# Performance work log

Hardware: AMD Instinct MI355X
Metric: run time of the kernel (lower is better)

Reference implementation:

```python
import jax, jax.numpy as jnp
import numpy as np

EPS_NORM = 1e-12   # F.normalize eps
EPS_Q = 1e-5       # quant scale clamp

def simple_rmsnorm(x):
    # F.normalize(x, dim=-1) * sqrt(dim)  ==  x / sqrt(mean(x^2))
    d = x.shape[-1]
    n = jnp.maximum(jnp.linalg.norm(x, axis=-1, keepdims=True), EPS_NORM)
    return x / n * jnp.sqrt(jnp.asarray(d, x.dtype))

def activation_quant(x):
    # per-token 8-bit absmax quant
    scale = 127.0 / jnp.clip(jnp.max(jnp.abs(x), axis=-1, keepdims=True), EPS_Q, None)
    return jnp.clip(jnp.round(x * scale), -128.0, 127.0) / scale

def weight_quant(w):
    # per-tensor ternary quant: scale = 1 / mean|w|
    scale = 1.0 / jnp.clip(jnp.mean(jnp.abs(w)), EPS_Q, None)
    return jnp.clip(jnp.round(w * scale), -1.0, 1.0) / scale

def bitlinear158(x, w):
    xn = simple_rmsnorm(x)
    # straight-through estimators
    xq = xn + jax.lax.stop_gradient(activation_quant(xn) - xn)
    wq = w + jax.lax.stop_gradient(weight_quant(w) - w)
    # w is [out, in] like nn.Linear
    return jnp.einsum('bsd,od->bso', xq, wq)

def setup_inputs() -> dict:
    key = jax.random.key(0)
    k1, k2, k3 = jax.random.split(key, 3)
    dim, inner = 2048, 8192
    x = jax.random.normal(k1, (4, 2048, dim), dtype=jnp.float32)
    w1 = jax.random.normal(k2, (inner, dim), dtype=jnp.float32) * 0.02
    w2 = jax.random.normal(k3, (dim, inner), dtype=jnp.float32) * 0.02
    return {"x": x, "w1": w1, "w2": w2}

def reference(x, w1, w2):
    h = bitlinear158(x, w1)
    h = jax.nn.gelu(h, approximate=False)  # nn.GELU() default = exact erf
    return bitlinear158(h, w2)
```

## Files before the change

### kernel.cpp

```cpp
#include <hip/hip_runtime.h>
#include <hip/hip_bf16.h>
#include <hip/hip_fp16.h>

typedef __attribute__((ext_vector_type(4))) int i32x4;
typedef __attribute__((ext_vector_type(8))) unsigned short u16x8;
typedef __attribute__((ext_vector_type(8))) char c8;
typedef __attribute__((ext_vector_type(4))) char c4;
typedef unsigned int u32;
typedef unsigned short u16;

#define SCH0() __builtin_amdgcn_sched_barrier(0)

__device__ __forceinline__ void gload_lds16(const void* g, void* l) {
  __builtin_amdgcn_global_load_lds((const u32 __attribute__((address_space(1)))*)g,
                                   (u32 __attribute__((address_space(3)))*)l, 16, 0, 0);
}
__device__ __forceinline__ float h2f(u16 u) { return __half2float(__ushort_as_half(u)); }
__device__ __forceinline__ u16  f2h(float f){ return __half_as_ushort(__float2half_rn(f)); }

__global__ __launch_bounds__(256) void prep_kernel(const float* __restrict__ x,
    char* __restrict__ qx, float* __restrict__ invs,
    const float* __restrict__ w1, const float* __restrict__ w2,
    double* __restrict__ part) {
  const int tid = threadIdx.x;
  __shared__ double sd[256];
  __shared__ float sf[256];
  if (blockIdx.x < 8192) {
    const int D = 2048;
    int row = blockIdx.x;
    const float* xr = x + (size_t)row * D;
    float4 a = ((const float4*)xr)[tid * 2], b = ((const float4*)xr)[tid * 2 + 1];
    float v[8] = {a.x, a.y, a.z, a.w, b.x, b.y, b.z, b.w};
    double ss = 0; float mx = 0.0f;
#pragma unroll
    for (int i = 0; i < 8; i++) { ss += (double)v[i] * v[i]; mx = fmaxf(mx, fabsf(v[i])); }
    sd[tid] = ss; sf[tid] = mx; __syncthreads();
    for (int o = 128; o > 0; o >>= 1) {
      if (tid < o) { sd[tid] += sd[tid + o]; sf[tid] = fmaxf(sf[tid], sf[tid + o]); }
      __syncthreads();
    }
    __shared__ float bn, bs;
    if (tid == 0) {
      float n = fmaxf((float)sqrt(sd[0]), 1e-12f);
      float amax = sf[0] * (sqrtf((float)D) / n);
      float cl = fmaxf(amax, 1e-5f);
      bn = n; bs = 127.0f / cl;
      invs[row] = cl / 127.0f;
    }
    __syncthreads();
    float n = bn, s = bs, sq = sqrtf((float)D);
    c8 q;
#pragma unroll
    for (int i = 0; i < 8; i++) {
      float xn = (v[i] / n) * sq;
      float r = rintf(xn * s);
      r = fminf(fmaxf(r, -128.0f), 127.0f);
      q[i] = (char)(int)r;
    }
    *(c8*)&qx[(size_t)row * D + tid * 8] = q;
  } else {
    const int n4 = 4194304;
    const bool isw2 = blockIdx.x >= 8704;
    const float* w = isw2 ? w2 : w1;
    const int vb = blockIdx.x - (isw2 ? 8704 : 8192);
    double s = 0;
    for (int i = vb * 256 + tid; i < n4; i += 512 * 256) {
      float4 v = ((const float4*)w)[i];
      s += (double)fabsf(v.x) + (double)fabsf(v.y) + (double)fabsf(v.z) + (double)fabsf(v.w);
    }
    sd[tid] = s; __syncthreads();
    for (int o = 128; o > 0; o >>= 1) { if (tid < o) sd[tid] += sd[tid + o]; __syncthreads(); }
    if (tid == 0) part[(isw2 ? 512 : 0) + vb] = sd[0];
  }
}

__global__ __launch_bounds__(256) void wscale_final(const double* __restrict__ part,
    float* __restrict__ wsc) {
  int tid = threadIdx.x;
  __shared__ double sd[256];
  sd[tid] = part[tid] + part[tid + 256]; __syncthreads();
  for (int o = 128; o > 0; o >>= 1) { if (tid < o) sd[tid] += sd[tid + o]; __syncthreads(); }
  double s1 = sd[0]; __syncthreads();
  sd[tid] = part[512 + tid] + part[768 + tid]; __syncthreads();
  for (int o = 128; o > 0; o >>= 1) { if (tid < o) sd[tid] += sd[tid + o]; __syncthreads(); }
  if (tid == 0) {
    float m1 = (float)(s1 / 16777216.0);
    float m2 = (float)(sd[0] / 16777216.0);
    float d1 = fmaxf(m1, 1e-5f), d2 = fmaxf(m2, 1e-5f);
    wsc[0] = 1.0f / d1; wsc[1] = d1; wsc[2] = 1.0f / d2; wsc[3] = d2;
  }
}

__global__ __launch_bounds__(256) void quant_w_kernel(const float* __restrict__ w1,
    char* __restrict__ q1, const float* __restrict__ w2, char* __restrict__ q2,
    const float* __restrict__ wsc) {
  const int n4 = 4194304;
  const bool isw2 = blockIdx.x >= 2048;
  const float* w = isw2 ? w2 : w1;
  char* q = isw2 ? q2 : q1;
  float s = isw2 ? wsc[2] : wsc[0];
  const int vb = blockIdx.x - (isw2 ? 2048 : 0);
  for (int i = vb * 256 + threadIdx.x; i < n4; i += 2048 * 256) {
    float4 v = ((const float4*)w)[i];
    c4 o;
    o[0] = (char)(int)(fminf(fmaxf(rintf(v.x * s), -1.0f), 1.0f));
    o[1] = (char)(int)(fminf(fmaxf(rintf(v.y * s), -1.0f), 1.0f));
    o[2] = (char)(int)(fminf(fmaxf(rintf(v.z * s), -1.0f), 1.0f));
    o[3] = (char)(int)(fminf(fmaxf(rintf(v.w * s), -1.0f), 1.0f));
    ((c4*)q)[i] = o;
  }
}

#define READ_A3(BUF, HALF, DST)                                            \
  { _Pragma("unroll") for (int f_ = 0; f_ < 4; f_++)                       \
      DST[f_] = *(const i32x4*)&sm[BUF][0][(wm * 128 + (HALF) * 64 + llo + f_ * 16) * 64 + koff]; }
#define READ_B3(BUF, HALF, DST)                                            \
  { _Pragma("unroll") for (int f_ = 0; f_ < 2; f_++)                       \
      DST[f_] = *(const i32x4*)&sm[BUF][1][(wn * 64 + (HALF) * 32 + llo + f_ * 16) * 64 + koff]; }
#define MMAQ(AV, BV, MH, NH)                                               \
  { __builtin_amdgcn_s_setprio(1);                                         \
    _Pragma("unroll") for (int m_ = 0; m_ < 4; m_++)                       \
      _Pragma("unroll") for (int n_ = 0; n_ < 2; n_++)                     \
        acc[(MH) * 4 + m_][(NH) * 2 + n_] =                                \
            __builtin_amdgcn_mfma_i32_16x16x64_i8(AV[m_], BV[n_],          \
                acc[(MH) * 4 + m_][(NH) * 2 + n_], 0, 0, 0);               \
    __builtin_amdgcn_s_setprio(0); }
#define STAGE3(BUF, KT)                                                    \
  { size_t ko_ = (size_t)(KT) * 64;                                        \
    gload_lds16(gA0 + ko_, &sm[BUF][0][tid * 16]);                         \
    gload_lds16(gB0 + ko_, &sm[BUF][1][tid * 16]);                         \
    gload_lds16(gA1 + ko_, &sm[BUF][0][8192 + tid * 16]);                  \
    gload_lds16(gB1 + ko_, &sm[BUF][1][8192 + tid * 16]); }
#define TILE_M(BR, BN, BS, KT)                                             \
  { STAGE3(BS, (KT) + 2);                                                  \
    SCH0();                                                                \
    READ_B3(BR, 1, bhi); SCH0();                                           \
    MMAQ(alo, blo, 0, 0); SCH0();                                          \
    READ_A3(BR, 1, ahi); SCH0();                                           \
    MMAQ(alo, bhi, 0, 1);                                                  \
    MMAQ(ahi, blo, 1, 0); SCH0();                                          \
    asm volatile("s_waitcnt vmcnt(4) lgkmcnt(0)\n\ts_barrier" ::: "memory"); \
    READ_A3(BN, 0, alo); READ_B3(BN, 0, blo); SCH0();                      \
    MMAQ(ahi, bhi, 1, 1); }

template <int EPI>
__global__ __launch_bounds__(512, 2) void gemm_i8(const char* __restrict__ A,
    const char* __restrict__ B, int N, int K, size_t ldA, size_t ldB, int gridN,
    const float* __restrict__ rowscale, const float* __restrict__ wsc,
    int widx, void* __restrict__ outp) {
  __shared__ __align__(16) char sm[3][2][16384];
  const int tid = threadIdx.x;
  const int lane = tid & 63, w = tid >> 6;
  const int wm = w >> 2, wn = w & 3;
  const int llo = lane & 15, lhi = lane >> 4;
  const int koff = ((lhi ^ ((llo >> 1) & 3)) << 4);

  const int nwg = gridDim.x, cpx = nwg >> 3;
  const int swz = (blockIdx.x & 7) * cpx + (blockIdx.x >> 3);
  const int band = gridN << 2;
  const int g = swz / band, idx = swz % band;
  const int bm = (g << 2) + (idx & 3), bn = idx >> 2;

  const int NT = K >> 6;
  const int NITER = (NT - 2) / 3;

  const int rs = tid >> 2;
  const int kbs = (((tid & 3) ^ ((tid >> 3) & 3)) << 4);
  const char* gA0 = A + (size_t)(bm * 256 + rs) * ldA + kbs;
  const char* gA1 = gA0 + (size_t)128 * ldA;
  const char* gB0 = B + (size_t)(bn * 256 + rs) * ldB + kbs;
  const char* gB1 = gB0 + (size_t)128 * ldB;

  i32x4 alo[4], ahi[4], blo[2], bhi[2];
  i32x4 acc[8][4];
#pragma unroll
  for (int m = 0; m < 8; m++)
#pragma unroll
    for (int n = 0; n < 4; n++) acc[m][n] = (i32x4){0, 0, 0, 0};

  STAGE3(0, 0);
  asm volatile("s_nop 0" ::: "memory");
  STAGE3(1, 1);
  asm volatile("s_waitcnt vmcnt(4)\n\ts_barrier" ::: "memory");
  READ_A3(0, 0, alo); READ_B3(0, 0, blo);

  for (int it = 0, t = 0; it < NITER; ++it, t += 3) {
    TILE_M(0, 1, 2, t);
    TILE_M(1, 2, 0, t + 1);
    TILE_M(2, 0, 1, t + 2);
  }
  {
    SCH0();
    READ_B3(0, 1, bhi); SCH0();
    MMAQ(alo, blo, 0, 0); SCH0();
    READ_A3(0, 1, ahi); SCH0();
    MMAQ(alo, bhi, 0, 1);
    MMAQ(ahi, blo, 1, 0); SCH0();
    asm volatile("s_waitcnt vmcnt(0) lgkmcnt(0)\n\ts_barrier" ::: "memory");
    READ_A3(1, 0, alo); READ_B3(1, 0, blo); SCH0();
    MMAQ(ahi, bhi, 1, 1);
  }
  {
    READ_B3(1, 1, bhi);
    MMAQ(alo, blo, 0, 0);
    READ_A3(1, 1, ahi);
    MMAQ(alo, bhi, 0, 1);
    MMAQ(ahi, blo, 1, 0);
    MMAQ(ahi, bhi, 1, 1);
  }

  float wdeq = wsc[widx];
#pragma unroll
  for (int mf = 0; mf < 8; mf++) {
#pragma unroll
    for (int reg = 0; reg < 4; reg++) {
      int r = bm * 256 + wm * 128 + mf * 16 + lhi * 4 + reg;
      float deq = rowscale[r] * wdeq;
#pragma unroll
      for (int nf = 0; nf < 4; nf++) {
        int c = bn * 256 + wn * 64 + nf * 16 + llo;
        float val = (float)acc[mf][nf][reg] * deq;
        if (EPI == 0) {
          float gg = 0.5f * val * (1.0f + erff(val * 0.70710678118654752440f));
          ((u16*)outp)[(size_t)r * N + c] = f2h(gg);
        } else {
          ((float*)outp)[(size_t)r * N + c] = val;
        }
      }
    }
  }
}

__global__ __launch_bounds__(256) void quant_h_kernel(u16* __restrict__ h, float* __restrict__ invs) {
  const int D = 8192;
  int row = blockIdx.x, tid = threadIdx.x;
  u16* hr = h + (size_t)row * D;
  float v[32];
#pragma unroll
  for (int j = 0; j < 4; j++) {
    u16x8 u = *(const u16x8*)&hr[j * 2048 + tid * 8];
#pragma unroll
    for (int e = 0; e < 8; e++) v[j * 8 + e] = h2f(u[e]);
  }
  double ss = 0; float mx = 0.0f;
#pragma unroll
  for (int i = 0; i < 32; i++) { ss += (double)v[i] * v[i]; mx = fmaxf(mx, fabsf(v[i])); }
  __shared__ double sd[256]; __shared__ float sf[256];
  sd[tid] = ss; sf[tid] = mx; __syncthreads();
  for (int o = 128; o > 0; o >>= 1) {
    if (tid < o) { sd[tid] += sd[tid + o]; sf[tid] = fmaxf(sf[tid], sf[tid + o]); }
    __syncthreads();
  }
  __shared__ float bn, bs;
  if (tid == 0) {
    float n = fmaxf((float)sqrt(sd[0]), 1e-12f);
    float amax = sf[0] * (sqrtf((float)D) / n);
    float cl = fmaxf(amax, 1e-5f);
    bn = n; bs = 127.0f / cl;
    invs[row] = cl / 127.0f;
  }
  __syncthreads();
  float n = bn, s = bs, sq = sqrtf((float)D);
  char* hq = (char*)hr;
#pragma unroll
  for (int j = 0; j < 4; j++) {
    c8 q;
#pragma unroll
    for (int e = 0; e < 8; e++) {
      float xn = (v[j * 8 + e] / n) * sq;
      float r = rintf(xn * s);
      r = fminf(fmaxf(r, -128.0f), 127.0f);
      q[e] = (char)(int)r;
    }
    *(c8*)&hq[j * 2048 + tid * 8] = q;
  }
}

extern "C" void kernel_launch(void* const* d_in, const int* in_sizes, int n_in,
                              void* d_out, int out_size, void* d_ws, size_t ws_size,
                              hipStream_t stream) {
  const float* x  = (const float*)d_in[0];
  const float* w1 = (const float*)d_in[1];
  const float* w2 = (const float*)d_in[2];

  char* ws = (char*)d_ws;
  char*   qx     = (char*)(ws + 0);
  char*   w1q    = (char*)(ws + 16777216);
  char*   w2q    = (char*)(ws + 33554432);
  u16*    h      = (u16*)(ws + 50331648);
  float*  invs_x = (float*)(ws + 184549376);
  float*  invs_h = (float*)(ws + 184582144);
  double* part   = (double*)(ws + 184614912);
  float*  wsc    = (float*)(ws + 184623104);

  prep_kernel<<<9216, 256, 0, stream>>>(x, qx, invs_x, w1, w2, part);
  wscale_final<<<1, 256, 0, stream>>>(part, wsc);
  quant_w_kernel<<<4096, 256, 0, stream>>>(w1, w1q, w2, w2q, wsc);
  gemm_i8<0><<<1024, 512, 0, stream>>>(qx, w1q, 8192, 2048, 2048, 2048, 32,
                                       invs_x, wsc, 1, (void*)h);
  quant_h_kernel<<<8192, 256, 0, stream>>>(h, invs_h);
  gemm_i8<1><<<256, 512, 0, stream>>>((const char*)h, w2q, 2048, 8192, 16384, 8192, 8,
                                      invs_h, wsc, 3, d_out);
}
```

Measured before the change: 421.7 us.

## Switch int8 GEMM to double-buffered 128-wide K tiles with 8-way swizzle

The int8 GEMM main loop moves from a triple-buffered 64-byte K step (prefetching two tiles ahead) to a double-buffered 128-byte K step that prefetches one tile ahead. The LDS swizzle widens from 4 to 8 16-byte chunks per row. The aim is to halve the number of barriers and loop iterations and to issue larger global-to-LDS copies. In exchange, each barrier waits on vmcnt(0), so the copy of the next tile has less time to overlap with compute, and LDS use grows from 96 KB to 128 KB per block.

Result: slower. 452.3 us (+7.3%).

```diff
diff --git a/kernel.cpp b/kernel.cpp
--- a/kernel.cpp
+++ b/kernel.cpp
@@ -111,36 +111,49 @@
   }
 }
 
-#define READ_A3(BUF, HALF, DST)                                            \
-  { _Pragma("unroll") for (int f_ = 0; f_ < 4; f_++)                       \
-      DST[f_] = *(const i32x4*)&sm[BUF][0][(wm * 128 + (HALF) * 64 + llo + f_ * 16) * 64 + koff]; }
-#define READ_B3(BUF, HALF, DST)                                            \
-  { _Pragma("unroll") for (int f_ = 0; f_ < 2; f_++)                       \
-      DST[f_] = *(const i32x4*)&sm[BUF][1][(wn * 64 + (HALF) * 32 + llo + f_ * 16) * 64 + koff]; }
-#define MMAQ(AV, BV, MH, NH)                                               \
-  { __builtin_amdgcn_s_setprio(1);                                         \
-    _Pragma("unroll") for (int m_ = 0; m_ < 4; m_++)                       \
-      _Pragma("unroll") for (int n_ = 0; n_ < 2; n_++)                     \
-        acc[(MH) * 4 + m_][(NH) * 2 + n_] =                                \
-            __builtin_amdgcn_mfma_i32_16x16x64_i8(AV[m_], BV[n_],          \
-                acc[(MH) * 4 + m_][(NH) * 2 + n_], 0, 0, 0);               \
+#define RD_A128(BUF, H, S, DST)                                             \
+  { _Pragma("unroll") for (int f_ = 0; f_ < 4; f_++)                        \
+      DST[f_] = *(const i32x4*)&sm[BUF][0][(wm * 128 + (H) * 64 + llo + f_ * 16) * 128 \
+                                           + (((((S) << 2) + lhi) ^ sw) << 4)]; }
+#define RD_B128(BUF, H, S, DST)                                             \
+  { _Pragma("unroll") for (int f_ = 0; f_ < 2; f_++)                        \
+      DST[f_] = *(const i32x4*)&sm[BUF][1][(wn * 64 + (H) * 32 + llo + f_ * 16) * 128 \
+                                           + (((((S) << 2) + lhi) ^ sw) << 4)]; }
+#define MMAQ(AV, BV, MH, NH)                                                \
+  { __builtin_amdgcn_s_setprio(1);                                          \
+    _Pragma("unroll") for (int m_ = 0; m_ < 4; m_++)                        \
+      _Pragma("unroll") for (int n_ = 0; n_ < 2; n_++)                      \
+        acc[(MH) * 4 + m_][(NH) * 2 + n_] =                                 \
+            __builtin_amdgcn_mfma_i32_16x16x64_i8(AV[m_], BV[n_],           \
+                acc[(MH) * 4 + m_][(NH) * 2 + n_], 0, 0, 0);                \
     __builtin_amdgcn_s_setprio(0); }
-#define STAGE3(BUF, KT)                                                    \
-  { size_t ko_ = (size_t)(KT) * 64;                                        \
-    gload_lds16(gA0 + ko_, &sm[BUF][0][tid * 16]);                         \
-    gload_lds16(gB0 + ko_, &sm[BUF][1][tid * 16]);                         \
-    gload_lds16(gA1 + ko_, &sm[BUF][0][8192 + tid * 16]);                  \
-    gload_lds16(gB1 + ko_, &sm[BUF][1][8192 + tid * 16]); }
-#define TILE_M(BR, BN, BS, KT)                                             \
-  { STAGE3(BS, (KT) + 2);                                                  \
-    SCH0();                                                                \
-    READ_B3(BR, 1, bhi); SCH0();                                           \
-    MMAQ(alo, blo, 0, 0); SCH0();                                          \
-    READ_A3(BR, 1, ahi); SCH0();                                           \
-    MMAQ(alo, bhi, 0, 1);                                                  \
-    MMAQ(ahi, blo, 1, 0); SCH0();                                          \
-    asm volatile("s_waitcnt vmcnt(4) lgkmcnt(0)\n\ts_barrier" ::: "memory"); \
-    READ_A3(BN, 0, alo); READ_B3(BN, 0, blo); SCH0();                      \
+#define STAGE128(BUF, KT)                                                   \
+  { size_t ko_ = (size_t)(KT) * 128;                                        \
+    gload_lds16(gA0 + ko_, &sm[BUF][0][tid * 16]);                          \
+    gload_lds16(gA1 + ko_, &sm[BUF][0][tid * 16 + 8192]);                   \
+    gload_lds16(gA2 + ko_, &sm[BUF][0][tid * 16 + 16384]);                  \
+    gload_lds16(gA3 + ko_, &sm[BUF][0][tid * 16 + 24576]);                  \
+    gload_lds16(gB0 + ko_, &sm[BUF][1][tid * 16]);                          \
+    gload_lds16(gB1 + ko_, &sm[BUF][1][tid * 16 + 8192]);                   \
+    gload_lds16(gB2 + ko_, &sm[BUF][1][tid * 16 + 16384]);                  \
+    gload_lds16(gB3 + ko_, &sm[BUF][1][tid * 16 + 24576]); }
+#define TILE128(C, T)                                                       \
+  { asm volatile("s_waitcnt vmcnt(0) lgkmcnt(0)\n\ts_barrier" ::: "memory");\
+    if ((T) + 1 < NT) STAGE128(C ^ 1, (T) + 1);                             \
+    SCH0();                                                                 \
+    RD_A128(C, 0, 0, alo); RD_B128(C, 0, 0, blo);                           \
+    RD_B128(C, 1, 0, bhi); SCH0();                                          \
+    MMAQ(alo, blo, 0, 0); SCH0();                                           \
+    RD_A128(C, 1, 0, ahi); SCH0();                                          \
+    MMAQ(alo, bhi, 0, 1);                                                   \
+    MMAQ(ahi, blo, 1, 0); SCH0();                                           \
+    RD_A128(C, 0, 1, alo); RD_B128(C, 0, 1, blo); SCH0();                   \
+    MMAQ(ahi, bhi, 1, 1);                                                   \
+    RD_B128(C, 1, 1, bhi); SCH0();                                          \
+    MMAQ(alo, blo, 0, 0); SCH0();                                           \
+    RD_A128(C, 1, 1, ahi); SCH0();                                          \
+    MMAQ(alo, bhi, 0, 1);                                                   \
+    MMAQ(ahi, blo, 1, 0); SCH0();                                           \
     MMAQ(ahi, bhi, 1, 1); }
 
 template <int EPI>
@@ -148,12 +161,12 @@
     const char* __restrict__ B, int N, int K, size_t ldA, size_t ldB, int gridN,
     const float* __restrict__ rowscale, const float* __restrict__ wsc,
     int widx, void* __restrict__ outp) {
-  __shared__ __align__(16) char sm[3][2][16384];
+  __shared__ __align__(16) char sm[2][2][32768];
   const int tid = threadIdx.x;
   const int lane = tid & 63, w = tid >> 6;
   const int wm = w >> 2, wn = w & 3;
   const int llo = lane & 15, lhi = lane >> 4;
-  const int koff = ((lhi ^ ((llo >> 1) & 3)) << 4);
+  const int sw = llo & 7;
 
   const int nwg = gridDim.x, cpx = nwg >> 3;
   const int swz = (blockIdx.x & 7) * cpx + (blockIdx.x >> 3);
@@ -161,15 +174,18 @@
   const int g = swz / band, idx = swz % band;
   const int bm = (g << 2) + (idx & 3), bn = idx >> 2;
 
-  const int NT = K >> 6;
-  const int NITER = (NT - 2) / 3;
-
-  const int rs = tid >> 2;
-  const int kbs = (((tid & 3) ^ ((tid >> 3) & 3)) << 4);
-  const char* gA0 = A + (size_t)(bm * 256 + rs) * ldA + kbs;
-  const char* gA1 = gA0 + (size_t)128 * ldA;
-  const char* gB0 = B + (size_t)(bn * 256 + rs) * ldB + kbs;
-  const char* gB1 = gB0 + (size_t)128 * ldB;
+  const int NT = K >> 7;
+
+  const int rs0 = tid >> 3;
+  const int kbsrc = (((tid & 7) ^ ((tid >> 3) & 7)) << 4);
+  const char* gA0 = A + (size_t)(bm * 256 + rs0) * ldA + kbsrc;
+  const char* gA1 = gA0 + (size_t)64 * ldA;
+  const char* gA2 = gA0 + (size_t)128 * ldA;
+  const char* gA3 = gA0 + (size_t)192 * ldA;
+  const char* gB0 = B + (size_t)(bn * 256 + rs0) * ldB + kbsrc;
+  const char* gB1 = gB0 + (size_t)64 * ldB;
+  const char* gB2 = gB0 + (size_t)128 * ldB;
+  const char* gB3 = gB0 + (size_t)192 * ldB;
 
   i32x4 alo[4], ahi[4], blo[2], bhi[2];
   i32x4 acc[8][4];
@@ -178,35 +194,11 @@
 #pragma unroll
     for (int n = 0; n < 4; n++) acc[m][n] = (i32x4){0, 0, 0, 0};
 
-  STAGE3(0, 0);
-  asm volatile("s_nop 0" ::: "memory");
-  STAGE3(1, 1);
-  asm volatile("s_waitcnt vmcnt(4)\n\ts_barrier" ::: "memory");
-  READ_A3(0, 0, alo); READ_B3(0, 0, blo);
-
-  for (int it = 0, t = 0; it < NITER; ++it, t += 3) {
-    TILE_M(0, 1, 2, t);
-    TILE_M(1, 2, 0, t + 1);
-    TILE_M(2, 0, 1, t + 2);
-  }
-  {
-    SCH0();
-    READ_B3(0, 1, bhi); SCH0();
-    MMAQ(alo, blo, 0, 0); SCH0();
-    READ_A3(0, 1, ahi); SCH0();
-    MMAQ(alo, bhi, 0, 1);
-    MMAQ(ahi, blo, 1, 0); SCH0();
-    asm volatile("s_waitcnt vmcnt(0) lgkmcnt(0)\n\ts_barrier" ::: "memory");
-    READ_A3(1, 0, alo); READ_B3(1, 0, blo); SCH0();
-    MMAQ(ahi, bhi, 1, 1);
-  }
-  {
-    READ_B3(1, 1, bhi);
-    MMAQ(alo, blo, 0, 0);
-    READ_A3(1, 1, ahi);
-    MMAQ(alo, bhi, 0, 1);
-    MMAQ(ahi, blo, 1, 0);
-    MMAQ(ahi, bhi, 1, 1);
+  STAGE128(0, 0);
+
+  for (int t = 0; t < NT; t += 2) {
+    TILE128(0, t);
+    TILE128(1, t + 1);
   }
 
   float wdeq = wsc[widx];
```
